# Performance work log

Measured on AMD Instinct MI355X. Metric: run time of the kernel, lower is better.

## Reference

```python
import jax, jax.numpy as jnp
import numpy as np

L, B, D = 2048, 4, 1024
H = 16
DK = D // 2            # q/k dim = 512
GLU_D = 2816
D_CONV = 4
NORMALIZER = 16.0
EPS = 1e-5


def setup_inputs() -> dict:
    key = jax.random.key(0)
    ks = jax.random.split(key, 20)
    s = 0.02
    inp = {
        "x": jax.random.normal(ks[0], (L, B, D), jnp.float32),
        "tn_w": jnp.ones((D,), jnp.float32),
        "tn_b": jnp.zeros((D,), jnp.float32),
        "conv_w": jax.random.normal(ks[1], (D, D_CONV), jnp.float32) * s,  # depthwise kernel (d, w)
        "q_w": jax.random.normal(ks[2], (D, DK), jnp.float32) * s,
        "kg_w": jax.random.normal(ks[3], (D, DK), jnp.float32) * s,
        "v_w": jax.random.normal(ks[4], (D, D), jnp.float32) * s,
        "g_w": jax.random.normal(ks[5], (D, D), jnp.float32) * s,
        "g_b": jnp.zeros((D,), jnp.float32),
        "out_w": jax.random.normal(ks[6], (D, D), jnp.float32) * s,
        "aug_balance": jax.random.normal(ks[7], (DK,), jnp.float32) * s,
        "cn_w": jnp.ones((D,), jnp.float32),
        "cn_b": jnp.zeros((D,), jnp.float32),
        "l1_w": jax.random.normal(ks[8], (D, GLU_D), jnp.float32) * s,
        "l2_w": jax.random.normal(ks[9], (D, GLU_D), jnp.float32) * s,
        "l3_w": jax.random.normal(ks[10], (GLU_D, D), jnp.float32) * s,
    }
    return inp


def _layernorm(y, w, b):
    m = jnp.mean(y, axis=-1, keepdims=True)
    v = jnp.var(y, axis=-1, keepdims=True)
    return (y - m) * jax.lax.rsqrt(v + EPS) * w + b


def _gla_scan(q, k, v, gk):
    # q,k,gk: (B,H,L,dk); v: (B,H,L,dv). Recurrent gated linear attention:
    # S_t = diag(exp(gk_t)) S_{t-1} + k_t v_t^T ; o_t = q_t S_t
    b, h, l, dk = q.shape
    dv = v.shape[-1]
    qT = jnp.moveaxis(q, 2, 0)  # (L,B,H,dk)
    kT = jnp.moveaxis(k, 2, 0)
    vT = jnp.moveaxis(v, 2, 0)
    gT = jnp.moveaxis(gk, 2, 0)

    def step(S, inp):
        q_t, k_t, v_t, g_t = inp
        S = jnp.exp(g_t)[..., None] * S + k_t[..., :, None] * v_t[..., None, :]
        o_t = jnp.einsum('bhk,bhkv->bhv', q_t, S)
        return S, o_t

    S0 = jnp.zeros((b, h, dk, dv), jnp.float32)
    _, o = jax.lax.scan(step, S0, (qT, kT, vT, gT))  # o: (L,B,H,dv)
    return jnp.moveaxis(o, 0, 2)  # (B,H,L,dv)


def reference(x, tn_w, tn_b, conv_w, q_w, kg_w, v_w, g_w, g_b, out_w,
              aug_balance, cn_w, cn_b, l1_w, l2_w, l3_w):
    residual = x  # (L,B,D)
    h = _layernorm(x, tn_w, tn_b)
    h = jnp.transpose(h, (1, 0, 2))  # (B,L,D)

    # causal depthwise conv1d (kernel 4, left pad 3) + SiLU
    hp = jnp.pad(h, ((0, 0), (D_CONV - 1, 0), (0, 0)))
    y = sum(hp[:, i:i + L, :] * conv_w[:, i] for i in range(D_CONV))
    y = jax.nn.silu(y)

    q = y @ q_w                     # (B,L,DK)
    kg = y @ kg_w                   # (B,L,DK)
    v = y @ v_w                     # (B,L,D)
    g = y @ g_w + g_b               # (B,L,D)

    gk = jax.nn.log_sigmoid(kg) / NORMALIZER
    k = 1.0 - jnp.exp(gk)

    dk_h = DK // H   # 32
    dv_h = D // H    # 64
    qh = q.reshape(B, L, H, dk_h).transpose(0, 2, 1, 3).astype(jnp.float32)
    kh = k.reshape(B, L, H, dk_h).transpose(0, 2, 1, 3).astype(jnp.float32)
    vh = v.reshape(B, L, H, dv_h).transpose(0, 2, 1, 3).astype(jnp.float32)
    gh = gk.reshape(B, L, H, dk_h).transpose(0, 2, 1, 3).astype(jnp.float32)
    aug = aug_balance.reshape(H, dk_h).astype(jnp.float32)

    o = _gla_scan(qh, kh, vh, gh)  # (B,H,L,dv_h)

    # self-augmentation term
    aug_w = jnp.einsum('bhld,hd,bhld->bhl', qh, aug, kh)
    o = o + jax.nn.sigmoid(aug_w[..., None] * vh)

    # group norm: LayerNorm over head dim, no affine
    m = jnp.mean(o, axis=-1, keepdims=True)
    var = jnp.var(o, axis=-1, keepdims=True)
    o = (o - m) * jax.lax.rsqrt(var + EPS)
    o = o.transpose(0, 2, 1, 3).reshape(B, L, D).astype(x.dtype)

    o = jax.nn.silu(g) * o
    o = o @ out_w                   # (B,L,D)

    x1 = jnp.transpose(o, (1, 0, 2)) + residual  # back to (L,B,D)

    z = _layernorm(x1, cn_w, cn_b)
    glu = (jax.nn.silu(z @ l1_w) * (z @ l2_w)) @ l3_w
    return glu + x1
```

## Files before the change

kernel.cpp:

```cpp
#include <hip/hip_runtime.h>


#define Lseq 2048
#define Bb 4
#define Dd 1024
#define Hh 16
#define GLUD 2816
#define NC 32
#define CHK 64

typedef float f32x4 __attribute__((ext_vector_type(4)));
typedef __bf16 bf16x8 __attribute__((ext_vector_type(8)));
typedef unsigned short u16;
typedef u16 u16x8 __attribute__((ext_vector_type(8)));

__device__ __forceinline__ u16 f2bf(float f) {
  unsigned int u = __float_as_uint(f);
  u += 0x7fffu + ((u >> 16) & 1u);
  return (u16)(u >> 16);
}
__device__ __forceinline__ float bf2f(u16 b) {
  return __uint_as_float(((unsigned int)b) << 16);
}

__device__ __forceinline__ int swz(int col, int row) {
  return (col & ~31) | ((((col >> 3) + (row >> 1)) & 3) << 3) | (col & 7);
}

__device__ __forceinline__ void gll16(const void* g, void* l) {
  __builtin_amdgcn_global_load_lds((const __attribute__((address_space(1))) void*)g,
                                   (__attribute__((address_space(3))) void*)l, 16, 0, 0);
}

__device__ __forceinline__ float block_sum(float v, float* red) {
#pragma unroll
  for (int o = 32; o > 0; o >>= 1) v += __shfl_down(v, o);
  __syncthreads();
  if ((threadIdx.x & 63) == 0) red[threadIdx.x >> 6] = v;
  __syncthreads();
  return red[0] + red[1] + red[2] + red[3];
}

__global__ __launch_bounds__(256) void ln1_k(const float* __restrict__ x,
                                             const float* __restrict__ w,
                                             const float* __restrict__ bia,
                                             float* __restrict__ h) {
  __shared__ float red[4];
  int r = blockIdx.x;
  int l = r >> 2, bb = r & 3;
  const float* xr = x + (size_t)r * Dd;
  int d0 = threadIdx.x * 4;
  float4 xv = *(const float4*)&xr[d0];
  float mean = block_sum(xv.x + xv.y + xv.z + xv.w, red) * (1.f / Dd);
  float a0 = xv.x - mean, a1 = xv.y - mean, a2 = xv.z - mean, a3 = xv.w - mean;
  float var = block_sum(a0 * a0 + a1 * a1 + a2 * a2 + a3 * a3, red) * (1.f / Dd);
  float rs = rsqrtf(var + 1e-5f);
  float4 ov;
  ov.x = a0 * rs * w[d0 + 0] + bia[d0 + 0];
  ov.y = a1 * rs * w[d0 + 1] + bia[d0 + 1];
  ov.z = a2 * rs * w[d0 + 2] + bia[d0 + 2];
  ov.w = a3 * rs * w[d0 + 3] + bia[d0 + 3];
  *(float4*)&h[((size_t)(bb * Lseq + l)) * Dd + d0] = ov;
}

__global__ __launch_bounds__(256) void ln2_k(const float* __restrict__ x1,
                                             const float* __restrict__ w,
                                             const float* __restrict__ bia,
                                             u16* __restrict__ z) {
  __shared__ float red[4];
  int r = blockIdx.x;
  const float* xr = x1 + (size_t)r * Dd;
  int d0 = threadIdx.x * 4;
  float4 xv = *(const float4*)&xr[d0];
  float mean = block_sum(xv.x + xv.y + xv.z + xv.w, red) * (1.f / Dd);
  float a0 = xv.x - mean, a1 = xv.y - mean, a2 = xv.z - mean, a3 = xv.w - mean;
  float var = block_sum(a0 * a0 + a1 * a1 + a2 * a2 + a3 * a3, red) * (1.f / Dd);
  float rs = rsqrtf(var + 1e-5f);
  ushort4 o;
  o.x = f2bf(a0 * rs * w[d0 + 0] + bia[d0 + 0]);
  o.y = f2bf(a1 * rs * w[d0 + 1] + bia[d0 + 1]);
  o.z = f2bf(a2 * rs * w[d0 + 2] + bia[d0 + 2]);
  o.w = f2bf(a3 * rs * w[d0 + 3] + bia[d0 + 3]);
  int dcol = (d0 & ~31) | ((((d0 >> 3) + (r >> 1)) & 3) << 3) | (d0 & 7);
  *(ushort4*)&z[(size_t)r * Dd + dcol] = o;
}

__global__ __launch_bounds__(256) void conv_k(const float* __restrict__ h,
                                              const float* __restrict__ cw,
                                              u16* __restrict__ ybf) {
  int m = blockIdx.x;
  int b = m >> 11, l = m & (Lseq - 1);
  int d0 = threadIdx.x * 4;
  float4 acc = {0.f, 0.f, 0.f, 0.f};
  const float* hb = h + ((size_t)b * Lseq) * Dd + d0;
#pragma unroll
  for (int w = 0; w < 4; w++) {
    int ll = l - 3 + w;
    if (ll >= 0) {
      float4 hv = *(const float4*)&hb[(size_t)ll * Dd];
      acc.x += hv.x * cw[(d0 + 0) * 4 + w];
      acc.y += hv.y * cw[(d0 + 1) * 4 + w];
      acc.z += hv.z * cw[(d0 + 2) * 4 + w];
      acc.w += hv.w * cw[(d0 + 3) * 4 + w];
    }
  }
  ushort4 o;
  o.x = f2bf(acc.x / (1.f + expf(-acc.x)));
  o.y = f2bf(acc.y / (1.f + expf(-acc.y)));
  o.z = f2bf(acc.z / (1.f + expf(-acc.z)));
  o.w = f2bf(acc.w / (1.f + expf(-acc.w)));
  int dcol = (d0 & ~31) | ((((d0 >> 3) + (m >> 1)) & 3) << 3) | (d0 & 7);
  *(ushort4*)&ybf[(size_t)m * Dd + dcol] = o;
}

__global__ __launch_bounds__(256) void prep_k(const float* __restrict__ q_w,
                                              const float* __restrict__ kg_w,
                                              const float* __restrict__ v_w,
                                              const float* __restrict__ g_w,
                                              const float* __restrict__ out_w,
                                              const float* __restrict__ l1_w,
                                              const float* __restrict__ l2_w,
                                              const float* __restrict__ l3_w,
                                              u16* __restrict__ Wqkvg,
                                              u16* __restrict__ Wout,
                                              u16* __restrict__ Wl12,
                                              u16* __restrict__ Wl3) {
  __shared__ float tile[32][33];
  int blk = blockIdx.x;
  const float* src;
  u16* dst;
  int R, C, ilv = 0, off = 0, base;
  if (blk < 512)       { src = q_w;   dst = Wqkvg;              R = 1024; C = 512;  base = 0; }
  else if (blk < 1024) { src = kg_w;  dst = Wqkvg + 512 * 1024; R = 1024; C = 512;  base = 512; }
  else if (blk < 2048) { src = v_w;   dst = Wqkvg + 1024 * 1024; R = 1024; C = 1024; base = 1024; }
  else if (blk < 3072) { src = g_w;   dst = Wqkvg + 2048 * 1024; R = 1024; C = 1024; base = 2048; }
  else if (blk < 4096) { src = out_w; dst = Wout;               R = 1024; C = 1024; base = 3072; }
  else if (blk < 6912) { src = l1_w;  dst = Wl12; R = 1024; C = 2816; ilv = 1; off = 0; base = 4096; }
  else if (blk < 9728) { src = l2_w;  dst = Wl12; R = 1024; C = 2816; ilv = 1; off = 1; base = 6912; }
  else                 { src = l3_w;  dst = Wl3;  R = 2816; C = 1024; base = 9728; }
  int local = blk - base;
  int ct = C >> 5;
  int bx = local % ct, by = local / ct;
  int tx = threadIdx.x & 31, ty = threadIdx.x >> 5;
  int c0 = bx * 32, r0 = by * 32;
#pragma unroll
  for (int k = 0; k < 4; k++)
    tile[ty + 8 * k][tx] = src[(size_t)(r0 + ty + 8 * k) * C + c0 + tx];
  __syncthreads();
#pragma unroll
  for (int k = 0; k < 4; k++) {
    int c = c0 + ty + 8 * k;
    int dstrow = ilv ? (((c >> 4) << 5) + off * 16 + (c & 15)) : c;
    int kpos = r0 + tx;
    dst[(size_t)dstrow * R + swz(kpos, dstrow)] = f2bf(tile[tx][ty + 8 * k]);
  }
}

__global__ __launch_bounds__(256) void passA_k(const float* __restrict__ decay,
                                               const u16* __restrict__ qkvg16,
                                               float* __restrict__ T,
                                               float* __restrict__ P) {
  int wave = threadIdx.x >> 6, lane = threadIdx.x & 63;
  int c = blockIdx.x * 4 + wave, bh = blockIdx.y;
  int b = bh >> 4, h = bh & 15;
  size_t t0 = (size_t)b * Lseq + c * CHK;
  const float* ep = decay + t0 * 512 + h * 32;
  const u16* vp = qkvg16 + t0 * 3072 + 1024 + h * 64 + lane;
  const float* dp = decay + t0 * 512 + h * 32 + (lane & 31);
  float S[32];
#pragma unroll
  for (int i = 0; i < 32; i++) S[i] = 0.f;
  float p = 1.f;
  u16 vnext = vp[0];
  float dnext = dp[0];
#pragma unroll 1
  for (int ts = 0; ts < CHK; ts++) {
    float vj = bf2f(vnext), dl = dnext;
    int tn = (ts + 1 < CHK) ? ts + 1 : ts;
    vnext = vp[(size_t)tn * 3072];
    dnext = dp[(size_t)tn * 512];
    const float* e = ep + (size_t)ts * 512;
    p *= dl;
#pragma unroll
    for (int i = 0; i < 32; i++) {
      float ei = e[i];
      float kv = (1.f - ei) * vj;
      S[i] = ei * S[i] + kv;
    }
  }
  float* Tc = T + ((size_t)bh * NC + c) * 2048;
#pragma unroll
  for (int i = 0; i < 32; i++) Tc[i * 64 + lane] = S[i];
  if (lane < 32) P[((size_t)bh * NC + c) * 32 + lane] = p;
}

__global__ __launch_bounds__(256) void passB_k(const float* __restrict__ T,
                                               const float* __restrict__ P,
                                               float* __restrict__ Sg) {
  int bh = blockIdx.x;
  int tid = threadIdx.x;
  int f = tid * 8, i = f >> 6;
  float s[8];
#pragma unroll
  for (int e = 0; e < 8; e++) s[e] = 0.f;
  for (int c = 0; c < NC; c++) {
    size_t base = ((size_t)bh * NC + c) * 2048 + f;
    float pc = P[((size_t)bh * NC + c) * 32 + i];
#pragma unroll
    for (int e = 0; e < 8; e++) {
      float tv = T[base + e];
      Sg[base + e] = s[e];
      s[e] = pc * s[e] + tv;
    }
  }
}

__global__ __launch_bounds__(256) void passC_k(const float* __restrict__ decay,
                                               const u16* __restrict__ qkvg16,
                                               const float* __restrict__ Sg,
                                               const float* __restrict__ aug,
                                               const float* __restrict__ gb,
                                               u16* __restrict__ o2) {
  int wave = threadIdx.x >> 6, lane = threadIdx.x & 63;
  int c = blockIdx.x * 4 + wave, bh = blockIdx.y;
  int b = bh >> 4, h = bh & 15;
  size_t t0 = (size_t)b * Lseq + c * CHK;
  const float* ep = decay + t0 * 512 + h * 32;
  const unsigned int* qp = (const unsigned int*)(qkvg16 + t0 * 3072 + h * 32);
  const u16* vp = qkvg16 + t0 * 3072 + 1024 + h * 64 + lane;
  const u16* gp = qkvg16 + t0 * 3072 + 2048 + h * 64 + lane;
  float S[32];
  const float* Sgc = Sg + ((size_t)bh * NC + c) * 2048;
#pragma unroll
  for (int i = 0; i < 32; i++) S[i] = Sgc[i * 64 + lane];
  float vaug[32];
#pragma unroll
  for (int i = 0; i < 32; i++) vaug[i] = aug[h * 32 + i];
  float gbv = gb[h * 64 + lane];
  int colbase = h * 64 + lane;
  int colfix = (colbase & ~31) | (colbase & 7);
  int colrot0 = colbase >> 3;
  u16 vnext = vp[0], gnext = gp[0];
#pragma unroll 1
  for (int ts = 0; ts < CHK; ts++) {
    float vj = bf2f(vnext);
    float gg = bf2f(gnext) + gbv;
    int tn = (ts + 1 < CHK) ? ts + 1 : ts;
    vnext = vp[(size_t)tn * 3072];
    gnext = gp[(size_t)tn * 3072];
    const float* e = ep + (size_t)ts * 512;
    const unsigned int* q = qp + (size_t)ts * 1536;
    float a0 = 0.f, a1 = 0.f, aw = 0.f;
#pragma unroll
    for (int i = 0; i < 32; i += 2) {
      unsigned int qq = q[i >> 1];
      float q0 = __uint_as_float(qq << 16);
      float q1 = __uint_as_float(qq & 0xffff0000u);
      float e0 = e[i], e1 = e[i + 1];
      float k0 = 1.f - e0, k1 = 1.f - e1;
      S[i + 0] = e0 * S[i + 0] + k0 * vj; a0 += q0 * S[i + 0];
      S[i + 1] = e1 * S[i + 1] + k1 * vj; a1 += q1 * S[i + 1];
      aw += q0 * vaug[i] * k0 + q1 * vaug[i + 1] * k1;
    }
    float o = (a0 + a1) + 1.f / (1.f + expf(-aw * vj));
    float s = o;
#pragma unroll
    for (int d = 1; d < 64; d <<= 1) s += __shfl_xor(s, d);
    float dcen = o - s * (1.f / 64.f);
    float ss = dcen * dcen;
#pragma unroll
    for (int d = 1; d < 64; d <<= 1) ss += __shfl_xor(ss, d);
    float rs = rsqrtf(ss * (1.f / 64.f) + 1e-5f);
    float res = (gg / (1.f + expf(-gg))) * dcen * rs;
    int m = (int)t0 + ts;
    int dcol = colfix | (((colrot0 + (m >> 1)) & 3) << 3);
    o2[(size_t)m * 1024 + dcol] = f2bf(res);
  }
}

template <int EPI>
__global__ __launch_bounds__(256) void gemm_bt(const u16* __restrict__ A,
                                               const u16* __restrict__ B,
                                               int M, int N, int K,
                                               float* __restrict__ Cf,
                                               const float* __restrict__ addsrc,
                                               u16* __restrict__ Cbf,
                                               float* __restrict__ decayp) {
  __shared__ __align__(16) u16 lA[2 * 4096];
  __shared__ __align__(16) u16 lB[2 * 4096];
  const int tid = threadIdx.x;
  const int wave = tid >> 6, lane = tid & 63;
  const int m0 = blockIdx.y * 128, n0 = blockIdx.x * 128;
  const int wm = wave & 1, wn = wave >> 1;
  f32x4 acc[4][4];
#pragma unroll
  for (int a = 0; a < 4; a++)
#pragma unroll
    for (int b = 0; b < 4; b++) acc[a][b] = {0.f, 0.f, 0.f, 0.f};

  const int srow = lane >> 2;
  const int sk8 = (lane & 3) * 8;
  const int rsel = lane & 15;
  const int rot = (((lane >> 4) + (rsel >> 1)) & 3) << 3;
  for (int k0 = 0; k0 < K; k0 += 64) {
    __syncthreads();
#pragma unroll
    for (int g = 0; g < 2; g++) {
#pragma unroll
      for (int it = 0; it < 2; it++) {
        int j = wave * 2 + it;
        int row = j * 16 + srow;
        gll16(A + (size_t)(m0 + row) * K + k0 + g * 32 + sk8, &lA[g * 4096 + j * 512]);
        gll16(B + (size_t)(n0 + row) * K + k0 + g * 32 + sk8, &lB[g * 4096 + j * 512]);
      }
    }
    __syncthreads();
#pragma unroll
    for (int g = 0; g < 2; g++) {
      bf16x8 af[4], bfr[4];
#pragma unroll
      for (int t = 0; t < 4; t++) {
        af[t] = __builtin_bit_cast(bf16x8,
                 *(const u16x8*)&lA[g * 4096 + (wm * 64 + t * 16 + rsel) * 32 + rot]);
        bfr[t] = __builtin_bit_cast(bf16x8,
                 *(const u16x8*)&lB[g * 4096 + (wn * 64 + t * 16 + rsel) * 32 + rot]);
      }
#pragma unroll
      for (int tm = 0; tm < 4; tm++)
#pragma unroll
        for (int tn = 0; tn < 4; tn++)
          acc[tm][tn] = __builtin_amdgcn_mfma_f32_16x16x32_bf16(af[tm], bfr[tn], acc[tm][tn], 0, 0, 0);
    }
  }

  const int rquad = (lane >> 4) * 4;
  const int csel = lane & 15;
#pragma unroll
  for (int tm = 0; tm < 4; tm++) {
    int rowb = m0 + wm * 64 + tm * 16 + rquad;
#pragma unroll
    for (int tn = 0; tn < 4; tn++) {
      int col = n0 + wn * 64 + tn * 16 + csel;
#pragma unroll
      for (int r = 0; r < 4; r++) {
        float v = acc[tm][tn][r];
        int row = rowb + r;
        if (EPI == 0) {
          if (col >= 512 && col < 1024) {
            float sg = 1.f / (1.f + expf(-v));
            decayp[(size_t)row * 512 + (col - 512)] = expf(0.0625f * logf(sg));
          } else {
            Cbf[(size_t)row * N + col] = f2bf(v);
          }
        } else if (EPI == 1) {
          int l = row & (Lseq - 1), bb = row >> 11;
          size_t o = ((size_t)(l * Bb + bb)) * Dd + col;
          Cf[o] = v + addsrc[o];
        } else if (EPI == 2) {
          size_t o = (size_t)row * Dd + col;
          Cf[o] = v + addsrc[o];
        } else {
          if ((tn & 1) == 0) {
            float u2 = acc[tm][tn + 1][r];
            float p = (v / (1.f + expf(-v))) * u2;
            int oc = (n0 >> 1) + wn * 32 + ((tn >> 1) << 4) + csel;
            Cbf[(size_t)row * (N >> 1) + swz(oc, row)] = f2bf(p);
          }
        }
      }
    }
  }
}

extern "C" void kernel_launch(void* const* d_in, const int* in_sizes, int n_in,
                              void* d_out, int out_size, void* d_ws, size_t ws_size,
                              hipStream_t stream) {
  const float* x = (const float*)d_in[0];
  const float* tn_w = (const float*)d_in[1];
  const float* tn_b = (const float*)d_in[2];
  const float* conv_w = (const float*)d_in[3];
  const float* q_w = (const float*)d_in[4];
  const float* kg_w = (const float*)d_in[5];
  const float* v_w = (const float*)d_in[6];
  const float* g_w = (const float*)d_in[7];
  const float* g_b = (const float*)d_in[8];
  const float* out_w = (const float*)d_in[9];
  const float* aug = (const float*)d_in[10];
  const float* cn_w = (const float*)d_in[11];
  const float* cn_b = (const float*)d_in[12];
  const float* l1_w = (const float*)d_in[13];
  const float* l2_w = (const float*)d_in[14];
  const float* l3_w = (const float*)d_in[15];
  float* out = (float*)d_out;
  char* ws = (char*)d_ws;

  u16* Wqkvg = (u16*)(ws + 0);
  u16* Wout = (u16*)(ws + 6291456);
  u16* Wl12 = (u16*)(ws + 8388608);
  u16* Wl3 = (u16*)(ws + 19922944);
  float* hbuf = (float*)(ws + 25690112);
  float* x1 = hbuf;
  u16* ybf = (u16*)(ws + 59244544);
  u16* o2bf = (u16*)(ws + 59244544);
  u16* qkvg16 = (u16*)(ws + 76021760);
  u16* zbf = (u16*)(ws + 76021760);
  u16* pbf = (u16*)(ws + 126353408);
  float* decay = (float*)(ws + 172490752);
  float* Tbuf = (float*)(ws + 189267968);
  float* Sg = Tbuf;
  float* Pbuf = (float*)(ws + 206045184);

  dim3 b256(256);
  prep_k<<<12544, b256, 0, stream>>>(q_w, kg_w, v_w, g_w, out_w, l1_w, l2_w, l3_w,
                                     Wqkvg, Wout, Wl12, Wl3);
  ln1_k<<<8192, b256, 0, stream>>>(x, tn_w, tn_b, hbuf);
  conv_k<<<8192, b256, 0, stream>>>(hbuf, conv_w, ybf);
  gemm_bt<0><<<dim3(24, 64), b256, 0, stream>>>(ybf, Wqkvg, 8192, 3072, 1024, nullptr, nullptr, qkvg16, decay);
  passA_k<<<dim3(NC / 4, 64), b256, 0, stream>>>(decay, qkvg16, Tbuf, Pbuf);
  passB_k<<<64, b256, 0, stream>>>(Tbuf, Pbuf, Sg);
  passC_k<<<dim3(NC / 4, 64), b256, 0, stream>>>(decay, qkvg16, Sg, aug, g_b, o2bf);
  gemm_bt<1><<<dim3(8, 64), b256, 0, stream>>>(o2bf, Wout, 8192, 1024, 1024, x1, x, nullptr, nullptr);
  ln2_k<<<8192, b256, 0, stream>>>(x1, cn_w, cn_b, zbf);
  gemm_bt<3><<<dim3(44, 64), b256, 0, stream>>>(zbf, Wl12, 8192, 5632, 1024, nullptr, nullptr, pbf, nullptr);
  gemm_bt<2><<<dim3(8, 64), b256, 0, stream>>>(pbf, Wl3, 8192, 1024, 2816, out, x1, nullptr, nullptr);
}
```

Before: 697.7 us.

## Store LN1 output as bf16, widen passB grid, use 128x64 tiles for N=1024 GEMMs

Several independent changes land together. LN1 now writes bf16 instead of fp32, which halves the traffic that conv_k reads, at some cost in precision before the convolution. passB is split across eight blocks per head so each thread scans one element, giving 512 blocks instead of 64. The out-projection and l3 GEMMs move to a new 128x64-tile kernel, doubling their block count to fill more CUs. Wave indices in passA and passC are made uniform via readfirstlane.

```diff
diff --git a/kernel.cpp b/kernel.cpp
--- a/kernel.cpp
+++ b/kernel.cpp
@@ -44,7 +44,7 @@
 __global__ __launch_bounds__(256) void ln1_k(const float* __restrict__ x,
                                              const float* __restrict__ w,
                                              const float* __restrict__ bia,
-                                             float* __restrict__ h) {
+                                             u16* __restrict__ h) {
   __shared__ float red[4];
   int r = blockIdx.x;
   int l = r >> 2, bb = r & 3;
@@ -55,12 +55,12 @@
   float a0 = xv.x - mean, a1 = xv.y - mean, a2 = xv.z - mean, a3 = xv.w - mean;
   float var = block_sum(a0 * a0 + a1 * a1 + a2 * a2 + a3 * a3, red) * (1.f / Dd);
   float rs = rsqrtf(var + 1e-5f);
-  float4 ov;
-  ov.x = a0 * rs * w[d0 + 0] + bia[d0 + 0];
-  ov.y = a1 * rs * w[d0 + 1] + bia[d0 + 1];
-  ov.z = a2 * rs * w[d0 + 2] + bia[d0 + 2];
-  ov.w = a3 * rs * w[d0 + 3] + bia[d0 + 3];
-  *(float4*)&h[((size_t)(bb * Lseq + l)) * Dd + d0] = ov;
+  ushort4 ov;
+  ov.x = f2bf(a0 * rs * w[d0 + 0] + bia[d0 + 0]);
+  ov.y = f2bf(a1 * rs * w[d0 + 1] + bia[d0 + 1]);
+  ov.z = f2bf(a2 * rs * w[d0 + 2] + bia[d0 + 2]);
+  ov.w = f2bf(a3 * rs * w[d0 + 3] + bia[d0 + 3]);
+  *(ushort4*)&h[((size_t)(bb * Lseq + l)) * Dd + d0] = ov;
 }
 
 __global__ __launch_bounds__(256) void ln2_k(const float* __restrict__ x1,
@@ -85,23 +85,23 @@
   *(ushort4*)&z[(size_t)r * Dd + dcol] = o;
 }
 
-__global__ __launch_bounds__(256) void conv_k(const float* __restrict__ h,
+__global__ __launch_bounds__(256) void conv_k(const u16* __restrict__ h,
                                               const float* __restrict__ cw,
                                               u16* __restrict__ ybf) {
   int m = blockIdx.x;
   int b = m >> 11, l = m & (Lseq - 1);
   int d0 = threadIdx.x * 4;
   float4 acc = {0.f, 0.f, 0.f, 0.f};
-  const float* hb = h + ((size_t)b * Lseq) * Dd + d0;
+  const u16* hb = h + ((size_t)b * Lseq) * Dd + d0;
 #pragma unroll
   for (int w = 0; w < 4; w++) {
     int ll = l - 3 + w;
     if (ll >= 0) {
-      float4 hv = *(const float4*)&hb[(size_t)ll * Dd];
-      acc.x += hv.x * cw[(d0 + 0) * 4 + w];
-      acc.y += hv.y * cw[(d0 + 1) * 4 + w];
-      acc.z += hv.z * cw[(d0 + 2) * 4 + w];
-      acc.w += hv.w * cw[(d0 + 3) * 4 + w];
+      ushort4 hv = *(const ushort4*)&hb[(size_t)ll * Dd];
+      acc.x += bf2f(hv.x) * cw[(d0 + 0) * 4 + w];
+      acc.y += bf2f(hv.y) * cw[(d0 + 1) * 4 + w];
+      acc.z += bf2f(hv.z) * cw[(d0 + 2) * 4 + w];
+      acc.w += bf2f(hv.w) * cw[(d0 + 3) * 4 + w];
     }
   }
   ushort4 o;
@@ -160,7 +160,8 @@
                                                const u16* __restrict__ qkvg16,
                                                float* __restrict__ T,
                                                float* __restrict__ P) {
-  int wave = threadIdx.x >> 6, lane = threadIdx.x & 63;
+  int wave = __builtin_amdgcn_readfirstlane((int)(threadIdx.x >> 6));
+  int lane = threadIdx.x & 63;
   int c = blockIdx.x * 4 + wave, bh = blockIdx.y;
   int b = bh >> 4, h = bh & 15;
   size_t t0 = (size_t)b * Lseq + c * CHK;
@@ -197,21 +198,16 @@
 __global__ __launch_bounds__(256) void passB_k(const float* __restrict__ T,
                                                const float* __restrict__ P,
                                                float* __restrict__ Sg) {
-  int bh = blockIdx.x;
-  int tid = threadIdx.x;
-  int f = tid * 8, i = f >> 6;
-  float s[8];
-#pragma unroll
-  for (int e = 0; e < 8; e++) s[e] = 0.f;
+  int bh = blockIdx.x >> 3;
+  int f = (blockIdx.x & 7) * 256 + threadIdx.x;
+  int i = f >> 6;
+  float s = 0.f;
   for (int c = 0; c < NC; c++) {
     size_t base = ((size_t)bh * NC + c) * 2048 + f;
     float pc = P[((size_t)bh * NC + c) * 32 + i];
-#pragma unroll
-    for (int e = 0; e < 8; e++) {
-      float tv = T[base + e];
-      Sg[base + e] = s[e];
-      s[e] = pc * s[e] + tv;
-    }
+    float tv = T[base];
+    Sg[base] = s;
+    s = pc * s + tv;
   }
 }
 
@@ -221,7 +217,8 @@
                                                const float* __restrict__ aug,
                                                const float* __restrict__ gb,
                                                u16* __restrict__ o2) {
-  int wave = threadIdx.x >> 6, lane = threadIdx.x & 63;
+  int wave = __builtin_amdgcn_readfirstlane((int)(threadIdx.x >> 6));
+  int lane = threadIdx.x & 63;
   int c = blockIdx.x * 4 + wave, bh = blockIdx.y;
   int b = bh >> 4, h = bh & 15;
   size_t t0 = (size_t)b * Lseq + c * CHK;
@@ -352,13 +349,6 @@
           } else {
             Cbf[(size_t)row * N + col] = f2bf(v);
           }
-        } else if (EPI == 1) {
-          int l = row & (Lseq - 1), bb = row >> 11;
-          size_t o = ((size_t)(l * Bb + bb)) * Dd + col;
-          Cf[o] = v + addsrc[o];
-        } else if (EPI == 2) {
-          size_t o = (size_t)row * Dd + col;
-          Cf[o] = v + addsrc[o];
         } else {
           if ((tn & 1) == 0) {
             float u2 = acc[tm][tn + 1][r];
@@ -366,6 +356,88 @@
             int oc = (n0 >> 1) + wn * 32 + ((tn >> 1) << 4) + csel;
             Cbf[(size_t)row * (N >> 1) + swz(oc, row)] = f2bf(p);
           }
+        }
+      }
+    }
+  }
+}
+
+template <int EPI>
+__global__ __launch_bounds__(256) void gemm_bt64(const u16* __restrict__ A,
+                                                 const u16* __restrict__ B,
+                                                 int M, int N, int K,
+                                                 float* __restrict__ Cf,
+                                                 const float* __restrict__ addsrc) {
+  __shared__ __align__(16) u16 lA[2 * 4096];
+  __shared__ __align__(16) u16 lB[2 * 2048];
+  const int tid = threadIdx.x;
+  const int wave = tid >> 6, lane = tid & 63;
+  const int m0 = blockIdx.y * 128, n0 = blockIdx.x * 64;
+  const int wm = wave & 1, wn = wave >> 1;
+  f32x4 acc[4][2];
+#pragma unroll
+  for (int a = 0; a < 4; a++)
+#pragma unroll
+    for (int b = 0; b < 2; b++) acc[a][b] = {0.f, 0.f, 0.f, 0.f};
+
+  const int srow = lane >> 2;
+  const int sk8 = (lane & 3) * 8;
+  const int rsel = lane & 15;
+  const int rot = (((lane >> 4) + (rsel >> 1)) & 3) << 3;
+  for (int k0 = 0; k0 < K; k0 += 64) {
+    __syncthreads();
+#pragma unroll
+    for (int g = 0; g < 2; g++) {
+#pragma unroll
+      for (int it = 0; it < 2; it++) {
+        int j = wave * 2 + it;
+        int row = j * 16 + srow;
+        gll16(A + (size_t)(m0 + row) * K + k0 + g * 32 + sk8, &lA[g * 4096 + j * 512]);
+      }
+      {
+        int row = wave * 16 + srow;
+        gll16(B + (size_t)(n0 + row) * K + k0 + g * 32 + sk8, &lB[g * 2048 + wave * 512]);
+      }
+    }
+    __syncthreads();
+#pragma unroll
+    for (int g = 0; g < 2; g++) {
+      bf16x8 af[4], bfr[2];
+#pragma unroll
+      for (int t = 0; t < 4; t++)
+        af[t] = __builtin_bit_cast(bf16x8,
+                 *(const u16x8*)&lA[g * 4096 + (wm * 64 + t * 16 + rsel) * 32 + rot]);
+#pragma unroll
+      for (int t = 0; t < 2; t++)
+        bfr[t] = __builtin_bit_cast(bf16x8,
+                 *(const u16x8*)&lB[g * 2048 + (wn * 32 + t * 16 + rsel) * 32 + rot]);
+#pragma unroll
+      for (int tm = 0; tm < 4; tm++)
+#pragma unroll
+        for (int tn = 0; tn < 2; tn++)
+          acc[tm][tn] = __builtin_amdgcn_mfma_f32_16x16x32_bf16(af[tm], bfr[tn], acc[tm][tn], 0, 0, 0);
+    }
+  }
+
+  const int rquad = (lane >> 4) * 4;
+  const int csel = lane & 15;
+#pragma unroll
+  for (int tm = 0; tm < 4; tm++) {
+    int rowb = m0 + wm * 64 + tm * 16 + rquad;
+#pragma unroll
+    for (int tn = 0; tn < 2; tn++) {
+      int col = n0 + wn * 32 + tn * 16 + csel;
+#pragma unroll
+      for (int r = 0; r < 4; r++) {
+        float v = acc[tm][tn][r];
+        int row = rowb + r;
+        if (EPI == 1) {
+          int l = row & (Lseq - 1), bb = row >> 11;
+          size_t o = ((size_t)(l * Bb + bb)) * Dd + col;
+          Cf[o] = v + addsrc[o];
+        } else {
+          size_t o = (size_t)row * Dd + col;
+          Cf[o] = v + addsrc[o];
         }
       }
     }
@@ -398,8 +470,8 @@
   u16* Wout = (u16*)(ws + 6291456);
   u16* Wl12 = (u16*)(ws + 8388608);
   u16* Wl3 = (u16*)(ws + 19922944);
-  float* hbuf = (float*)(ws + 25690112);
-  float* x1 = hbuf;
+  u16* hbuf = (u16*)(ws + 25690112);
+  float* x1 = (float*)(ws + 25690112);
   u16* ybf = (u16*)(ws + 59244544);
   u16* o2bf = (u16*)(ws + 59244544);
   u16* qkvg16 = (u16*)(ws + 76021760);
@@ -417,10 +489,10 @@
   conv_k<<<8192, b256, 0, stream>>>(hbuf, conv_w, ybf);
   gemm_bt<0><<<dim3(24, 64), b256, 0, stream>>>(ybf, Wqkvg, 8192, 3072, 1024, nullptr, nullptr, qkvg16, decay);
   passA_k<<<dim3(NC / 4, 64), b256, 0, stream>>>(decay, qkvg16, Tbuf, Pbuf);
-  passB_k<<<64, b256, 0, stream>>>(Tbuf, Pbuf, Sg);
+  passB_k<<<512, b256, 0, stream>>>(Tbuf, Pbuf, Sg);
   passC_k<<<dim3(NC / 4, 64), b256, 0, stream>>>(decay, qkvg16, Sg, aug, g_b, o2bf);
-  gemm_bt<1><<<dim3(8, 64), b256, 0, stream>>>(o2bf, Wout, 8192, 1024, 1024, x1, x, nullptr, nullptr);
+  gemm_bt64<1><<<dim3(16, 64), b256, 0, stream>>>(o2bf, Wout, 8192, 1024, 1024, x1, x);
   ln2_k<<<8192, b256, 0, stream>>>(x1, cn_w, cn_b, zbf);
   gemm_bt<3><<<dim3(44, 64), b256, 0, stream>>>(zbf, Wl12, 8192, 5632, 1024, nullptr, nullptr, pbf, nullptr);
-  gemm_bt<2><<<dim3(8, 64), b256, 0, stream>>>(pbf, Wl3, 8192, 1024, 2816, out, x1, nullptr, nullptr);
-}
+  gemm_bt64<2><<<dim3(16, 64), b256, 0, stream>>>(pbf, Wl3, 8192, 1024, 2816, out, x1);
+}
```

Result: no change. 695.0 us (-0.4%).
